# Performance work log

Hardware: AMD Instinct MI355X
Metric: run time of the kernel (lower is better)

Reference implementation:

```python
import jax, jax.numpy as jnp
import numpy as np

NUM_HEADS = 8
IN_CH = 512
SCALING = float(IN_CH // 8) ** (-0.5)  # 0.125, as in the torch module


def _conv1x1(x, w, b):
    # x: [B,C,H,W], w: [O,C], b: [O]  (1x1 conv == channel matmul)
    return jnp.einsum('bchw,oc->bohw', x, w) + b[None, :, None, None]


def setup_inputs() -> dict:
    key = jax.random.key(0)
    ks = jax.random.split(key, 9)
    B, C, H, W = 4, IN_CH, 96, 96
    q = jax.random.normal(ks[0], (B, C, H, W), jnp.float32)
    v = jax.random.normal(ks[1], (B, C, H, W), jnp.float32)
    # xavier_uniform for [C,C] 1x1 conv weights
    limit = float(np.sqrt(6.0 / (C + C)))
    Wq = jax.random.uniform(ks[2], (C, C), jnp.float32, -limit, limit)
    Wk = jax.random.uniform(ks[3], (C, C), jnp.float32, -limit, limit)
    Wv = jax.random.uniform(ks[4], (C, C), jnp.float32, -limit, limit)
    bq = jnp.zeros((C,), jnp.float32)
    bk = jnp.zeros((C,), jnp.float32)
    bv = jnp.zeros((C,), jnp.float32)
    # gamma is init to 0 in the module; use a nonzero value so the output is nontrivial
    gamma = jax.random.normal(ks[5], (1,), jnp.float32) * 0.1
    return {'q': q, 'v': v, 'Wq': Wq, 'bq': bq, 'Wk': Wk, 'bk': bk,
            'Wv': Wv, 'bv': bv, 'gamma': gamma}


def reference(q, v, Wq, bq, Wk, bk, Wv, bv, gamma):
    B, C, H, W = q.shape
    nh = NUM_HEADS
    hd = C // nh
    t = _conv1x1(q, Wq, bq) * SCALING           # proj_query
    f = _conv1x1(q, Wk, bk)                     # proj_key
    g = _conv1x1(v, Wv, bv)                     # proj_value
    t = t.reshape(B * nh, hd, H, W)
    f = f.reshape(B * nh, hd, H, W)
    g = g.reshape(B * nh, hd, H, W)
    # criss-cross affinity: row (same y, all x') and column (same x, all y'!=y)
    e_row = jnp.einsum('bdyx,bdyi->byxi', t, f)  # [Bh, H, W, W]
    e_col = jnp.einsum('bdyx,bdix->byxi', t, f)  # [Bh, H, W, H]
    # exclude the current position from the column branch (CUDA kernel skips i==y)
    diag = (jnp.arange(H)[:, None, None] == jnp.arange(H)[None, None, :])  # [H,1,H]
    e_col = jnp.where(diag, -jnp.inf, e_col)
    attn = jax.nn.softmax(jnp.concatenate([e_row, e_col], axis=-1), axis=-1)  # [Bh,H,W,W+H]
    a_row, a_col = attn[..., :W], attn[..., W:]
    out = (jnp.einsum('byxi,bdyi->bdyx', a_row, g)
           + jnp.einsum('byxi,bdix->bdyx', a_col, g))  # [Bh, hd, H, W]
    out = out.reshape(B, C, H, W)
    return gamma[0] * out + v
```

## Files before the change

kernel.cpp:

```cpp
#include <hip/hip_runtime.h>
#include <hip/hip_bf16.h>

typedef __bf16 bf16;
typedef __attribute__((ext_vector_type(8))) __bf16 bf16x8;
typedef __attribute__((ext_vector_type(4))) float floatx4;

#define B_  4
#define C_  512
#define H_  96
#define W_  96
#define HD_ 64
#define HW_ 9216
#define BH_ 32
#define SCALING_ 0.125f
#define BHS_ 589824

static constexpr size_t T_ELEMS = (size_t)BH_ * HD_ * HW_;
static constexpr size_t S_ELEMS = (size_t)BH_ * HW_;

__global__ __launch_bounds__(256) void cast_qv(
    const float* __restrict__ q, const float* __restrict__ v,
    const float* __restrict__ Wq, const float* __restrict__ Wk, const float* __restrict__ Wv,
    bf16* __restrict__ qbT, bf16* __restrict__ vbT, bf16* __restrict__ Wb)
{
    const int z = blockIdx.z;
    const int tid = threadIdx.x;

    if (z == 8) {
        const int bi = blockIdx.y * 144 + blockIdx.x;
        if (bi < 768) {
            const int i  = bi * 256 + tid;
            const int e0 = i * 4;
            const int arr = e0 >> 18;
            const int off = e0 & 262143;
            const float* W = (arr == 0) ? Wq : (arr == 1) ? Wk : Wv;
            const float4 val = *(const float4*)(W + off);
            bf16 tmp[4] __attribute__((aligned(8)));
            tmp[0] = (bf16)val.x; tmp[1] = (bf16)val.y;
            tmp[2] = (bf16)val.z; tmp[3] = (bf16)val.w;
            *(uint2*)(Wb + e0) = *(const uint2*)tmp;
        }
        return;
    }

    const int s = z >> 2, b = z & 3;
    const float* sb = (s ? v : q) + (size_t)b * C_ * HW_;
    bf16*       db = (s ? vbT : qbT) + (size_t)b * HW_ * C_;
    const int p0 = blockIdx.x * 64, c0 = blockIdx.y * 64;

    __shared__ float ts[64][65];

    for (int i = tid; i < 1024; i += 256) {
        const int row = i >> 4, seg = i & 15;
        const float4 val = *(const float4*)(sb + (size_t)(c0 + row) * HW_ + p0 + seg * 4);
        ts[row][seg * 4 + 0] = val.x; ts[row][seg * 4 + 1] = val.y;
        ts[row][seg * 4 + 2] = val.z; ts[row][seg * 4 + 3] = val.w;
    }
    __syncthreads();
    for (int i = tid; i < 512; i += 256) {
        const int prow = i >> 3, cseg = i & 7;
        bf16 tmp[8] __attribute__((aligned(16)));
        #pragma unroll
        for (int k = 0; k < 8; k++) tmp[k] = (bf16)ts[cseg * 8 + k][prow];
        *(uint4*)(db + (size_t)(p0 + prow) * C_ + c0 + cseg * 8) = *(const uint4*)tmp;
    }
}

__device__ __forceinline__ void stage_swz(
    const bf16* __restrict__ A, const bf16* __restrict__ Bsrc,
    int o0, int p0, int k0, int tid, bf16* As, bf16* Bs)
{
    #pragma unroll
    for (int c = tid; c < 512; c += 256) {
        const int sc = c ^ ((c >> 3) & 7);
        const int row = sc >> 2, seg = sc & 3;
        const bf16* gA = A    + (size_t)(o0 + row) * C_ + k0 + seg * 8;
        const bf16* gB = Bsrc + (size_t)(p0 + row) * C_ + k0 + seg * 8;
#if __has_builtin(__builtin_amdgcn_global_load_lds)
        char* lA = (char*)As + (size_t)(c & ~63) * 16;
        char* lB = (char*)Bs + (size_t)(c & ~63) * 16;
        __builtin_amdgcn_global_load_lds((const __attribute__((address_space(1))) void*)gA,
                                         (__attribute__((address_space(3))) void*)lA, 16, 0, 0);
        __builtin_amdgcn_global_load_lds((const __attribute__((address_space(1))) void*)gB,
                                         (__attribute__((address_space(3))) void*)lB, 16, 0, 0);
#else
        *(uint4*)((char*)As + (size_t)c * 16) = *(const uint4*)gA;
        *(uint4*)((char*)Bs + (size_t)c * 16) = *(const uint4*)gB;
#endif
    }
}

__device__ __forceinline__ int swz_chunk(int r, int quad)
{
    return (r * 4 + quad) ^ ((r >> 1) & 7);
}

__device__ __forceinline__ void compute_swz(
    const bf16* As, const bf16* Bs,
    int mrow, int ncol, int l16, int quad, floatx4 acc[4][4])
{
    bf16x8 af[4], bf_[4];
    #pragma unroll
    for (int i = 0; i < 4; i++)
        af[i] = *(const bf16x8*)&As[swz_chunk(mrow + i * 16 + l16, quad) * 8];
    #pragma unroll
    for (int j = 0; j < 4; j++)
        bf_[j] = *(const bf16x8*)&Bs[swz_chunk(ncol + j * 16 + l16, quad) * 8];
    #pragma unroll
    for (int i = 0; i < 4; i++)
        #pragma unroll
        for (int j = 0; j < 4; j++)
            acc[i][j] = __builtin_amdgcn_mfma_f32_16x16x32_bf16(af[i], bf_[j], acc[i][j], 0, 0, 0);
}

__global__ __launch_bounds__(256) void conv_mfma(
    const bf16* __restrict__ Wb,
    const float* __restrict__ bq, const float* __restrict__ bk, const float* __restrict__ bv,
    const bf16* __restrict__ qbT, const bf16* __restrict__ vbT,
    bf16* __restrict__ tR, bf16* __restrict__ fR, bf16* __restrict__ g)
{
    const int z = blockIdx.z, arr = z >> 2, b = z & 3;
    const bf16* A    = Wb + (size_t)arr * C_ * C_;
    const bf16* Bsrc = ((arr == 2) ? vbT : qbT) + (size_t)b * HW_ * C_;
    const float* bias = (arr == 0) ? bq : (arr == 1) ? bk : bv;
    const float scale = (arr == 0) ? SCALING_ : 1.0f;

    const int p0 = blockIdx.x * 128;
    const int o0 = blockIdx.y * 128;

    __shared__ __align__(16) bf16 smem[17408];
    bf16* const As0 = smem;
    bf16* const Bs0 = smem + 4096;
    bf16* const As1 = smem + 8192;
    bf16* const Bs1 = smem + 12288;

    const int tid = threadIdx.x, lane = tid & 63;
    const int wave = tid >> 6, l16 = lane & 15, quad = lane >> 4;
    const int mrow = (wave >> 1) * 64, ncol = (wave & 1) * 64;

    floatx4 acc[4][4] = {};

    stage_swz(A, Bsrc, o0, p0, 0, tid, As0, Bs0);
    __syncthreads();

    for (int k0 = 0; k0 < C_; k0 += 64) {
        if (k0 + 32 < C_) stage_swz(A, Bsrc, o0, p0, k0 + 32, tid, As1, Bs1);
        compute_swz(As0, Bs0, mrow, ncol, l16, quad, acc);
        __syncthreads();
        if (k0 + 64 < C_) stage_swz(A, Bsrc, o0, p0, k0 + 64, tid, As0, Bs0);
        compute_swz(As1, Bs1, mrow, ncol, l16, quad, acc);
        __syncthreads();
    }

    if (arr < 2) {
        #pragma unroll
        for (int i = 0; i < 4; i++)
            #pragma unroll
            for (int r = 0; r < 4; r++) {
                const int ol_ = mrow + i * 16 + quad * 4 + r;
                const float bi = bias[o0 + ol_];
                #pragma unroll
                for (int j = 0; j < 4; j++) {
                    const int pl = ncol + j * 16 + l16;
                    smem[pl * 128 + (ol_ ^ ((pl & 7) << 3))] = (bf16)((acc[i][j][r] + bi) * scale);
                }
            }
        __syncthreads();
        bf16* dst = (arr == 0) ? tR : fR;
        #pragma unroll
        for (int c = tid; c < 2048; c += 256) {
            const int pl = c >> 4, oo = c & 15;
            const int pg = p0 + pl;
            const int y = pg / 96, x = pg - y * 96;
            const int og = o0 + oo * 8;
            const int bh = b * 8 + (og >> 6), d = og & 63;
            const size_t di = (size_t)bh * BHS_ + (size_t)y * 6144 + x * 64 + d;
            *(uint4*)(dst + di) = *(const uint4*)&smem[pl * 128 + ((oo ^ (pl & 7)) * 8)];
        }
    } else {
        const int TS = 136;
        #pragma unroll
        for (int i = 0; i < 4; i++)
            #pragma unroll
            for (int r = 0; r < 4; r++) {
                const int ol_ = mrow + i * 16 + quad * 4 + r;
                const float bi = bias[o0 + ol_];
                #pragma unroll
                for (int j = 0; j < 4; j++) {
                    const int pl = ncol + j * 16 + l16;
                    smem[ol_ * TS + pl] = (bf16)(acc[i][j][r] + bi);
                }
            }
        __syncthreads();
        #pragma unroll
        for (int c = tid; c < 2048; c += 256) {
            const int ol_ = c >> 4, po = c & 15;
            const size_t di = (size_t)(b * 512 + o0 + ol_) * HW_ + p0 + po * 8;
            *(uint4*)(g + di) = *(const uint4*)&smem[ol_ * TS + po * 8];
        }
    }
}

__global__ __launch_bounds__(256) void transpose_g(const bf16* __restrict__ src, bf16* __restrict__ dst)
{
    const int plane = blockIdx.y;
    const int y0 = blockIdx.x * 32;
    const bf16* s = src + (size_t)plane * HW_;
    bf16*       d = dst + (size_t)plane * HW_;

    __shared__ bf16 ts[32][100];
    const int tid = threadIdx.x;

    #pragma unroll
    for (int i = tid; i < 768; i += 256) {
        const int row = i / 24, seg = i % 24;
        *(uint2*)&ts[row][seg * 4] = *(const uint2*)(s + (size_t)(y0 + row) * W_ + seg * 4);
    }
    __syncthreads();
    #pragma unroll
    for (int i = tid; i < 768; i += 256) {
        const int x = i >> 3, yseg = i & 7;
        bf16 tmp[4] __attribute__((aligned(8)));
        #pragma unroll
        for (int k = 0; k < 4; k++) tmp[k] = ts[yseg * 4 + k][x];
        *(uint2*)(d + (size_t)x * H_ + y0 + yseg * 4) = *(const uint2*)tmp;
    }
}

__global__ __launch_bounds__(512) void attn_col(
    const bf16* __restrict__ tR, const bf16* __restrict__ fR, const bf16* __restrict__ gT,
    bf16* __restrict__ outC, float* __restrict__ mc, float* __restrict__ lc)
{
    const int x = blockIdx.x;
    const int bh = blockIdx.y;

    __shared__ __align__(16) bf16 tl[96][72];
    __shared__ __align__(16) bf16 fl[96][72];
    __shared__ __align__(16) bf16 el[96][104];

    const int tid = threadIdx.x;
    const size_t sbase = (size_t)bh * BHS_;

    for (int i = tid; i < 768; i += 512) {
        const int y = i >> 3, oct = i & 7;
        const size_t gi = sbase + (size_t)y * 6144 + (size_t)x * 64 + oct * 8;
        *(uint4*)&tl[y][oct * 8] = *(const uint4*)(tR + gi);
        *(uint4*)&fl[y][oct * 8] = *(const uint4*)(fR + gi);
    }
    __syncthreads();

    const int lane = tid & 63, wave = tid >> 6;
    const int l16 = lane & 15, quad = lane >> 4;

    __builtin_amdgcn_s_setprio(1);
    #pragma unroll
    for (int it = 0; it < 5; it++) {
        const int idx = wave + it * 8;
        if (idx < 36) {
            const int mt = idx / 6, nt = idx % 6;
            floatx4 a = {};
            #pragma unroll
            for (int ks = 0; ks < 2; ks++) {
                bf16x8 af = *(const bf16x8*)&tl[mt * 16 + l16][ks * 32 + quad * 8];
                bf16x8 bf_ = *(const bf16x8*)&fl[nt * 16 + l16][ks * 32 + quad * 8];
                a = __builtin_amdgcn_mfma_f32_16x16x32_bf16(af, bf_, a, 0, 0, 0);
            }
            #pragma unroll
            for (int r = 0; r < 4; r++) {
                const int row = mt * 16 + quad * 4 + r, col = nt * 16 + l16;
                el[row][col] = (row == col) ? (bf16)(-1e30f) : (bf16)a[r];
            }
        }
    }
    __builtin_amdgcn_s_setprio(0);
    __syncthreads();

    bf16 (*gl)[104] = (bf16 (*)[104])fl;
    const size_t gbase = sbase + (size_t)x * 96;
    for (int i = tid; i < 768; i += 512) {
        const int d = i / 12, seg = i % 12;
        *(uint4*)&gl[d][seg * 8] = *(const uint4*)(gT + gbase + (size_t)d * HW_ + seg * 8);
    }

    if (tid < 384) {
        const int r = tid >> 2, qu = tid & 3;
        float vals[24];
        float m = -1e30f;
        #pragma unroll
        for (int k = 0; k < 3; k++) {
            bf16x8 v8 = *(const bf16x8*)&el[r][qu * 24 + k * 8];
            #pragma unroll
            for (int e = 0; e < 8; e++) { vals[k * 8 + e] = (float)v8[e]; m = fmaxf(m, vals[k * 8 + e]); }
        }
        m = fmaxf(m, __shfl_xor(m, 1));
        m = fmaxf(m, __shfl_xor(m, 2));
        float s = 0.f;
        #pragma unroll
        for (int k = 0; k < 3; k++) {
            bf16 tmp[8] __attribute__((aligned(16)));
            #pragma unroll
            for (int e = 0; e < 8; e++) {
                const float p = __expf(vals[k * 8 + e] - m);
                s += p; tmp[e] = (bf16)p;
            }
            *(uint4*)&el[r][qu * 24 + k * 8] = *(const uint4*)tmp;
        }
        s += __shfl_xor(s, 1);
        s += __shfl_xor(s, 2);
        if (qu == 0) {
            mc[(size_t)bh * HW_ + x * 96 + r] = m;
            lc[(size_t)bh * HW_ + x * 96 + r] = s;
        }
    }
    __syncthreads();

    bf16 (*ol)[72] = tl;
    __builtin_amdgcn_s_setprio(1);
    #pragma unroll
    for (int it = 0; it < 3; it++) {
        const int idx = wave + it * 8;
        const int mt = idx >> 2, nt = idx & 3;
        floatx4 a = {};
        #pragma unroll
        for (int ks = 0; ks < 3; ks++) {
            bf16x8 pf = *(const bf16x8*)&el[mt * 16 + l16][ks * 32 + quad * 8];
            bf16x8 gf = *(const bf16x8*)&gl[nt * 16 + l16][ks * 32 + quad * 8];
            a = __builtin_amdgcn_mfma_f32_16x16x32_bf16(pf, gf, a, 0, 0, 0);
        }
        #pragma unroll
        for (int r = 0; r < 4; r++)
            ol[mt * 16 + quad * 4 + r][nt * 16 + l16] = (bf16)a[r];
    }
    __builtin_amdgcn_s_setprio(0);
    __syncthreads();

    bf16* ob = outC + sbase + (size_t)x * 6144;
    for (int i = tid; i < 768; i += 512) {
        const int j = i >> 3, oct = i & 7;
        *(uint4*)(ob + (size_t)j * 64 + oct * 8) = *(const uint4*)&ol[j][oct * 8];
    }
}

__global__ __launch_bounds__(512) void attn_row_merge(
    const bf16* __restrict__ tR, const bf16* __restrict__ fR, const bf16* __restrict__ g,
    const bf16* __restrict__ outC, const float* __restrict__ mc, const float* __restrict__ lc,
    const float* __restrict__ v, const float* __restrict__ gamma, float* __restrict__ out)
{
    const int y = blockIdx.x;
    const int bh = blockIdx.y;

    __shared__ __align__(16) bf16 tl[96][72];
    __shared__ __align__(16) bf16 fl[96][72];
    __shared__ __align__(16) bf16 el[96][104];
    __shared__ float mll[96], lll[96], wrl[96], wcl[96];

    const int tid = threadIdx.x;
    const size_t sbase = (size_t)bh * BHS_;
    const size_t slice = sbase + (size_t)y * 6144;

    for (int i = tid; i < 768; i += 512) {
        const int j = i >> 3, oct = i & 7;
        *(uint4*)&tl[j][oct * 8] = *(const uint4*)(tR + slice + (size_t)j * 64 + oct * 8);
        *(uint4*)&fl[j][oct * 8] = *(const uint4*)(fR + slice + (size_t)j * 64 + oct * 8);
    }

    uint4 oc0, oc1 = {};
    {
        const int xx = tid >> 3, oct = tid & 7;
        oc0 = *(const uint4*)(outC + sbase + (size_t)xx * 6144 + (size_t)y * 64 + oct * 8);
    }
    if (tid < 256) {
        const int i1 = tid + 512, xx = i1 >> 3, oct = i1 & 7;
        oc1 = *(const uint4*)(outC + sbase + (size_t)xx * 6144 + (size_t)y * 64 + oct * 8);
    }
    float4 vpA, vpB = {}, vpC, vpD = {};
    {
        const int d = tid / 12, xf = tid - d * 12;
        const size_t ob = sbase + (size_t)d * HW_ + (size_t)y * 96 + xf * 4;
        vpA = *(const float4*)(v + ob);
        vpC = *(const float4*)(v + ob + 48);
    }
    if (tid < 256) {
        const int j = tid + 512;
        const int d = j / 12, xf = j - d * 12;
        const size_t ob = sbase + (size_t)d * HW_ + (size_t)y * 96 + xf * 4;
        vpB = *(const float4*)(v + ob);
        vpD = *(const float4*)(v + ob + 48);
    }
    float mcv = 0.f, lcv = 0.f;
    if (tid < 96) {
        mcv = mc[(size_t)bh * HW_ + tid * 96 + y];
        lcv = lc[(size_t)bh * HW_ + tid * 96 + y];
    }
    __syncthreads();

    const int lane = tid & 63, wave = tid >> 6;
    const int l16 = lane & 15, quad = lane >> 4;

    __builtin_amdgcn_s_setprio(1);
    #pragma unroll
    for (int it = 0; it < 5; it++) {
        const int idx = wave + it * 8;
        if (idx < 36) {
            const int mt = idx / 6, nt = idx % 6;
            floatx4 a = {};
            #pragma unroll
            for (int ks = 0; ks < 2; ks++) {
                bf16x8 af = *(const bf16x8*)&tl[mt * 16 + l16][ks * 32 + quad * 8];
                bf16x8 bf_ = *(const bf16x8*)&fl[nt * 16 + l16][ks * 32 + quad * 8];
                a = __builtin_amdgcn_mfma_f32_16x16x32_bf16(af, bf_, a, 0, 0, 0);
            }
            #pragma unroll
            for (int r = 0; r < 4; r++)
                el[mt * 16 + quad * 4 + r][nt * 16 + l16] = (bf16)a[r];
        }
    }
    __builtin_amdgcn_s_setprio(0);
    __syncthreads();

    bf16 (*gl)[104] = (bf16 (*)[104])tl;
    const size_t gbase = sbase + (size_t)y * 96;
    for (int i = tid; i < 768; i += 512) {
        const int d = i / 12, seg = i % 12;
        *(uint4*)&gl[d][seg * 8] = *(const uint4*)(g + gbase + (size_t)d * HW_ + seg * 8);
    }

    bf16 (*ocl)[72] = fl;
    {
        const int xx = tid >> 3, oct = tid & 7;
        *(uint4*)&ocl[xx][oct * 8] = oc0;
    }
    if (tid < 256) {
        const int i1 = tid + 512, xx = i1 >> 3, oct = i1 & 7;
        *(uint4*)&ocl[xx][oct * 8] = oc1;
    }

    if (tid < 384) {
        const int r = tid >> 2, qu = tid & 3;
        float vals[24];
        float m = -1e30f;
        #pragma unroll
        for (int k = 0; k < 3; k++) {
            bf16x8 v8 = *(const bf16x8*)&el[r][qu * 24 + k * 8];
            #pragma unroll
            for (int e = 0; e < 8; e++) { vals[k * 8 + e] = (float)v8[e]; m = fmaxf(m, vals[k * 8 + e]); }
        }
        m = fmaxf(m, __shfl_xor(m, 1));
        m = fmaxf(m, __shfl_xor(m, 2));
        float s = 0.f;
        #pragma unroll
        for (int k = 0; k < 3; k++) {
            bf16 tmp[8] __attribute__((aligned(16)));
            #pragma unroll
            for (int e = 0; e < 8; e++) {
                const float p = __expf(vals[k * 8 + e] - m);
                s += p; tmp[e] = (bf16)p;
            }
            *(uint4*)&el[r][qu * 24 + k * 8] = *(const uint4*)tmp;
        }
        s += __shfl_xor(s, 1);
        s += __shfl_xor(s, 2);
        if (qu == 0) { mll[r] = m; lll[r] = s; }
    }
    __syncthreads();

    if (tid < 96) {
        const float mrv = mll[tid], lrv = lll[tid];
        const float mm = fmaxf(mrv, mcv);
        const float wr = __expf(mrv - mm), wc = __expf(mcv - mm);
        const float dn = lrv * wr + lcv * wc;
        wrl[tid] = wr / dn;
        wcl[tid] = wc / dn;
    }
    floatx4 pa[3] = {};
    __builtin_amdgcn_s_setprio(1);
    #pragma unroll
    for (int it = 0; it < 3; it++) {
        const int idx = wave + it * 8;
        const int mt = idx >> 2, nt = idx & 3;
        #pragma unroll
        for (int ks = 0; ks < 3; ks++) {
            bf16x8 pf = *(const bf16x8*)&el[mt * 16 + l16][ks * 32 + quad * 8];
            bf16x8 gf = *(const bf16x8*)&gl[nt * 16 + l16][ks * 32 + quad * 8];
            pa[it] = __builtin_amdgcn_mfma_f32_16x16x32_bf16(pf, gf, pa[it], 0, 0, 0);
        }
    }
    __builtin_amdgcn_s_setprio(0);
    __syncthreads();

    #pragma unroll
    for (int it = 0; it < 3; it++) {
        const int idx = wave + it * 8;
        const int mt = idx >> 2, nt = idx & 3;
        #pragma unroll
        for (int r = 0; r < 4; r++)
            el[mt * 16 + quad * 4 + r][nt * 16 + l16] = (bf16)pa[it][r];
    }
    __syncthreads();

    const float gam = gamma[0];
    float* stage = (float*)&tl[0][0];

    #pragma unroll
    for (int h = 0; h < 2; h++) {
        const int xbase = h * 48;
        #pragma unroll
        for (int s = 0; s < 6; s++) {
            const int j = tid + s * 512;
            const int r = j >> 6, d = j & 63;
            const int xx = xbase + r;
            stage[r * 65 + d] = (float)el[xx][d] * wrl[xx] + (float)ocl[xx][d] * wcl[xx];
        }
        __syncthreads();
        {
            const int d = tid / 12, xf = tid - d * 12;
            float4 o4;
            o4.x = stage[(xf * 4 + 0) * 65 + d];
            o4.y = stage[(xf * 4 + 1) * 65 + d];
            o4.z = stage[(xf * 4 + 2) * 65 + d];
            o4.w = stage[(xf * 4 + 3) * 65 + d];
            const float4 vp = h ? vpC : vpA;
            float4 rr;
            rr.x = gam * o4.x + vp.x; rr.y = gam * o4.y + vp.y;
            rr.z = gam * o4.z + vp.z; rr.w = gam * o4.w + vp.w;
            const size_t ob = sbase + (size_t)d * HW_ + (size_t)y * 96 + xbase + xf * 4;
            *(float4*)(out + ob) = rr;
        }
        if (tid < 256) {
            const int j = tid + 512;
            const int d = j / 12, xf = j - d * 12;
            float4 o4;
            o4.x = stage[(xf * 4 + 0) * 65 + d];
            o4.y = stage[(xf * 4 + 1) * 65 + d];
            o4.z = stage[(xf * 4 + 2) * 65 + d];
            o4.w = stage[(xf * 4 + 3) * 65 + d];
            const float4 vp = h ? vpD : vpB;
            float4 rr;
            rr.x = gam * o4.x + vp.x; rr.y = gam * o4.y + vp.y;
            rr.z = gam * o4.z + vp.z; rr.w = gam * o4.w + vp.w;
            const size_t ob = sbase + (size_t)d * HW_ + (size_t)y * 96 + xbase + xf * 4;
            *(float4*)(out + ob) = rr;
        }
        __syncthreads();
    }
}

extern "C" void kernel_launch(void* const* d_in, const int* in_sizes, int n_in,
                              void* d_out, int out_size, void* d_ws, size_t ws_size,
                              hipStream_t stream)
{
    const float* q     = (const float*)d_in[0];
    const float* v     = (const float*)d_in[1];
    const float* Wq    = (const float*)d_in[2];
    const float* bq    = (const float*)d_in[3];
    const float* Wk    = (const float*)d_in[4];
    const float* bk    = (const float*)d_in[5];
    const float* Wv    = (const float*)d_in[6];
    const float* bv    = (const float*)d_in[7];
    const float* gamma = (const float*)d_in[8];
    float* out = (float*)d_out;

    char* w = (char*)d_ws;
    const size_t Tb = T_ELEMS * sizeof(bf16);
    bf16* qbT  = (bf16*)(w + 0 * Tb);
    bf16* vbT  = (bf16*)(w + 1 * Tb);
    bf16* tR   = (bf16*)(w + 2 * Tb);
    bf16* fR   = (bf16*)(w + 3 * Tb);
    bf16* g    = (bf16*)(w + 4 * Tb);
    bf16* gT   = (bf16*)(w + 1 * Tb);
    bf16* outC = (bf16*)(w + 0 * Tb);
    bf16* Wb   = (bf16*)(w + 6 * Tb);
    float* mc  = (float*)(w + 6 * Tb + 1572864);
    float* lc  = mc + S_ELEMS;

    cast_qv <<<dim3(144, 8, 9), 256, 0, stream>>>(q, v, Wq, Wk, Wv, qbT, vbT, Wb);
    conv_mfma<<<dim3(72, 4, 12), 256, 0, stream>>>(Wb, bq, bk, bv, qbT, vbT, tR, fR, g);
    transpose_g<<<dim3(3, 2048), 256, 0, stream>>>(g, gT);
    attn_col<<<dim3(96, BH_), 512, 0, stream>>>(tR, fR, gT, outC, mc, lc);
    attn_row_merge<<<dim3(96, BH_), 512, 0, stream>>>(tR, fR, g, outC, mc, lc, v, gamma, out);
}
```

Before: 379.9 us.

## Enlarge conv GEMM tiles to 256x256 with 8 waves and deeper async LDS pipeline

```diff
diff --git a/kernel.cpp b/kernel.cpp
--- a/kernel.cpp
+++ b/kernel.cpp
@@ -66,54 +66,27 @@
     }
 }
 
-__device__ __forceinline__ void stage_swz(
-    const bf16* __restrict__ A, const bf16* __restrict__ Bsrc,
-    int o0, int p0, int k0, int tid, bf16* As, bf16* Bs)
-{
-    #pragma unroll
-    for (int c = tid; c < 512; c += 256) {
+__device__ __forceinline__ int swz_chunk(int r, int quad)
+{
+    return (r * 4 + quad) ^ ((r >> 1) & 7);
+}
+
+__device__ __forceinline__ void stage_half(
+    const bf16* __restrict__ src, int row0, int k0, int tid, bf16* dst)
+{
+    #pragma unroll
+    for (int it = 0; it < 2; ++it) {
+        const int c  = tid + it * 512;
         const int sc = c ^ ((c >> 3) & 7);
         const int row = sc >> 2, seg = sc & 3;
-        const bf16* gA = A    + (size_t)(o0 + row) * C_ + k0 + seg * 8;
-        const bf16* gB = Bsrc + (size_t)(p0 + row) * C_ + k0 + seg * 8;
-#if __has_builtin(__builtin_amdgcn_global_load_lds)
-        char* lA = (char*)As + (size_t)(c & ~63) * 16;
-        char* lB = (char*)Bs + (size_t)(c & ~63) * 16;
-        __builtin_amdgcn_global_load_lds((const __attribute__((address_space(1))) void*)gA,
-                                         (__attribute__((address_space(3))) void*)lA, 16, 0, 0);
-        __builtin_amdgcn_global_load_lds((const __attribute__((address_space(1))) void*)gB,
-                                         (__attribute__((address_space(3))) void*)lB, 16, 0, 0);
-#else
-        *(uint4*)((char*)As + (size_t)c * 16) = *(const uint4*)gA;
-        *(uint4*)((char*)Bs + (size_t)c * 16) = *(const uint4*)gB;
-#endif
-    }
-}
-
-__device__ __forceinline__ int swz_chunk(int r, int quad)
-{
-    return (r * 4 + quad) ^ ((r >> 1) & 7);
-}
-
-__device__ __forceinline__ void compute_swz(
-    const bf16* As, const bf16* Bs,
-    int mrow, int ncol, int l16, int quad, floatx4 acc[4][4])
-{
-    bf16x8 af[4], bf_[4];
-    #pragma unroll
-    for (int i = 0; i < 4; i++)
-        af[i] = *(const bf16x8*)&As[swz_chunk(mrow + i * 16 + l16, quad) * 8];
-    #pragma unroll
-    for (int j = 0; j < 4; j++)
-        bf_[j] = *(const bf16x8*)&Bs[swz_chunk(ncol + j * 16 + l16, quad) * 8];
-    #pragma unroll
-    for (int i = 0; i < 4; i++)
-        #pragma unroll
-        for (int j = 0; j < 4; j++)
-            acc[i][j] = __builtin_amdgcn_mfma_f32_16x16x32_bf16(af[i], bf_[j], acc[i][j], 0, 0, 0);
-}
-
-__global__ __launch_bounds__(256) void conv_mfma(
+        const bf16* gp = src + (size_t)(row0 + row) * C_ + k0 + seg * 8;
+        char* lp = (char*)dst + (size_t)(c & ~63) * 16;
+        __builtin_amdgcn_global_load_lds((const __attribute__((address_space(1))) void*)gp,
+                                         (__attribute__((address_space(3))) void*)lp, 16, 0, 0);
+    }
+}
+
+__global__ __launch_bounds__(512, 2) void conv_mfma(
     const bf16* __restrict__ Wb,
     const float* __restrict__ bq, const float* __restrict__ bk, const float* __restrict__ bv,
     const bf16* __restrict__ qbT, const bf16* __restrict__ vbT,
@@ -125,78 +98,124 @@
     const float* bias = (arr == 0) ? bq : (arr == 1) ? bk : bv;
     const float scale = (arr == 0) ? SCALING_ : 1.0f;
 
-    const int p0 = blockIdx.x * 128;
-    const int o0 = blockIdx.y * 128;
-
-    __shared__ __align__(16) bf16 smem[17408];
-    bf16* const As0 = smem;
-    bf16* const Bs0 = smem + 4096;
-    bf16* const As1 = smem + 8192;
-    bf16* const Bs1 = smem + 12288;
+    const int p0 = blockIdx.x * 256;
+    const int o0 = blockIdx.y * 256;
+
+    __shared__ __align__(16) bf16 smem[65536];
 
     const int tid = threadIdx.x, lane = tid & 63;
     const int wave = tid >> 6, l16 = lane & 15, quad = lane >> 4;
-    const int mrow = (wave >> 1) * 64, ncol = (wave & 1) * 64;
-
-    floatx4 acc[4][4] = {};
-
-    stage_swz(A, Bsrc, o0, p0, 0, tid, As0, Bs0);
-    __syncthreads();
-
-    for (int k0 = 0; k0 < C_; k0 += 64) {
-        if (k0 + 32 < C_) stage_swz(A, Bsrc, o0, p0, k0 + 32, tid, As1, Bs1);
-        compute_swz(As0, Bs0, mrow, ncol, l16, quad, acc);
-        __syncthreads();
-        if (k0 + 64 < C_) stage_swz(A, Bsrc, o0, p0, k0 + 64, tid, As0, Bs0);
-        compute_swz(As1, Bs1, mrow, ncol, l16, quad, acc);
-        __syncthreads();
-    }
+    const int wr = wave >> 2, wc = wave & 3;
+
+    floatx4 acc[8][4] = {};
+
+    stage_half(A,    o0, 0,   tid, smem + 0);
+    stage_half(Bsrc, p0, 0,   tid, smem + 16384);
+    stage_half(A,    o0, 32,  tid, smem + 8192);
+    stage_half(Bsrc, p0, 32,  tid, smem + 24576);
+    stage_half(A,    o0, 64,  tid, smem + 32768);
+    stage_half(Bsrc, p0, 64,  tid, smem + 49152);
+
+    #pragma unroll
+    for (int t = 0; t < 8; t++) {
+        #pragma unroll
+        for (int qp = 0; qp < 4; qp++) {
+            if (qp == 0) {
+                if (t == 7) asm volatile("s_waitcnt vmcnt(0)" ::: "memory");
+                else        asm volatile("s_waitcnt vmcnt(4)" ::: "memory");
+                __builtin_amdgcn_sched_barrier(0);
+            }
+            __builtin_amdgcn_s_barrier();
+            __builtin_amdgcn_sched_barrier(0);
+
+            const int mg = qp & 1, ks = qp >> 1;
+            const bf16* Ak = smem + (size_t)(t & 1) * 32768 + (size_t)ks * 8192;
+            const bf16* Bk = Ak + 16384;
+
+            bf16x8 af[4], bf_[4];
+            #pragma unroll
+            for (int i = 0; i < 4; i++) {
+                const int r = wr * 128 + mg * 64 + i * 16 + l16;
+                af[i] = *(const bf16x8*)&Ak[swz_chunk(r, quad) * 8];
+            }
+            #pragma unroll
+            for (int j = 0; j < 4; j++) {
+                const int r = wc * 64 + j * 16 + l16;
+                bf_[j] = *(const bf16x8*)&Bk[swz_chunk(r, quad) * 8];
+            }
+
+            if (qp == 0 && t + 1 < 8)
+                stage_half(A,    o0, (t + 1) * 64 + 32, tid,
+                           smem + (size_t)((t + 1) & 1) * 32768 + 8192);
+            if (qp == 1 && t + 1 < 8)
+                stage_half(Bsrc, p0, (t + 1) * 64 + 32, tid,
+                           smem + (size_t)((t + 1) & 1) * 32768 + 24576);
+            if (qp == 2 && t + 2 < 8)
+                stage_half(A,    o0, (t + 2) * 64, tid,
+                           smem + (size_t)(t & 1) * 32768);
+            if (qp == 3 && t + 2 < 8)
+                stage_half(Bsrc, p0, (t + 2) * 64, tid,
+                           smem + (size_t)(t & 1) * 32768 + 16384);
+
+            asm volatile("s_waitcnt lgkmcnt(0)" ::: "memory");
+            __builtin_amdgcn_sched_barrier(0);
+
+            __builtin_amdgcn_s_setprio(1);
+            #pragma unroll
+            for (int i = 0; i < 4; i++)
+                #pragma unroll
+                for (int j = 0; j < 4; j++)
+                    acc[mg * 4 + i][j] =
+                        __builtin_amdgcn_mfma_f32_16x16x32_bf16(af[i], bf_[j], acc[mg * 4 + i][j], 0, 0, 0);
+            __builtin_amdgcn_s_setprio(0);
+        }
+    }
+    __syncthreads();
 
     if (arr < 2) {
         #pragma unroll
-        for (int i = 0; i < 4; i++)
-            #pragma unroll
-            for (int r = 0; r < 4; r++) {
-                const int ol_ = mrow + i * 16 + quad * 4 + r;
+        for (int mi = 0; mi < 8; mi++)
+            #pragma unroll
+            for (int rr = 0; rr < 4; rr++) {
+                const int ol_ = wr * 128 + mi * 16 + quad * 4 + rr;
                 const float bi = bias[o0 + ol_];
                 #pragma unroll
                 for (int j = 0; j < 4; j++) {
-                    const int pl = ncol + j * 16 + l16;
-                    smem[pl * 128 + (ol_ ^ ((pl & 7) << 3))] = (bf16)((acc[i][j][r] + bi) * scale);
+                    const int pl = wc * 64 + j * 16 + l16;
+                    smem[pl * 256 + (ol_ ^ ((pl & 7) << 3))] = (bf16)((acc[mi][j][rr] + bi) * scale);
                 }
             }
         __syncthreads();
         bf16* dst = (arr == 0) ? tR : fR;
         #pragma unroll
-        for (int c = tid; c < 2048; c += 256) {
-            const int pl = c >> 4, oo = c & 15;
+        for (int c = tid; c < 8192; c += 512) {
+            const int pl = c >> 5, oo = c & 31;
             const int pg = p0 + pl;
             const int y = pg / 96, x = pg - y * 96;
             const int og = o0 + oo * 8;
             const int bh = b * 8 + (og >> 6), d = og & 63;
             const size_t di = (size_t)bh * BHS_ + (size_t)y * 6144 + x * 64 + d;
-            *(uint4*)(dst + di) = *(const uint4*)&smem[pl * 128 + ((oo ^ (pl & 7)) * 8)];
+            *(uint4*)(dst + di) = *(const uint4*)&smem[pl * 256 + ((oo * 8) ^ ((pl & 7) << 3))];
         }
     } else {
-        const int TS = 136;
-        #pragma unroll
-        for (int i = 0; i < 4; i++)
-            #pragma unroll
-            for (int r = 0; r < 4; r++) {
-                const int ol_ = mrow + i * 16 + quad * 4 + r;
+        #pragma unroll
+        for (int mi = 0; mi < 8; mi++)
+            #pragma unroll
+            for (int rr = 0; rr < 4; rr++) {
+                const int ol_ = wr * 128 + mi * 16 + quad * 4 + rr;
                 const float bi = bias[o0 + ol_];
                 #pragma unroll
                 for (int j = 0; j < 4; j++) {
-                    const int pl = ncol + j * 16 + l16;
-                    smem[ol_ * TS + pl] = (bf16)(acc[i][j][r] + bi);
+                    const int pl = wc * 64 + j * 16 + l16;
+                    smem[ol_ * 256 + (pl ^ ((ol_ & 7) << 3))] = (bf16)(acc[mi][j][rr] + bi);
                 }
             }
         __syncthreads();
         #pragma unroll
-        for (int c = tid; c < 2048; c += 256) {
-            const int ol_ = c >> 4, po = c & 15;
+        for (int c = tid; c < 8192; c += 512) {
+            const int ol_ = c >> 5, po = c & 31;
             const size_t di = (size_t)(b * 512 + o0 + ol_) * HW_ + p0 + po * 8;
-            *(uint4*)(g + di) = *(const uint4*)&smem[ol_ * TS + po * 8];
+            *(uint4*)(g + di) = *(const uint4*)&smem[ol_ * 256 + ((po * 8) ^ ((ol_ & 7) << 3))];
         }
     }
 }
@@ -574,7 +593,7 @@
     float* lc  = mc + S_ELEMS;
 
     cast_qv <<<dim3(144, 8, 9), 256, 0, stream>>>(q, v, Wq, Wk, Wv, qbT, vbT, Wb);
-    conv_mfma<<<dim3(72, 4, 12), 256, 0, stream>>>(Wb, bq, bk, bv, qbT, vbT, tR, fR, g);
+    conv_mfma<<<dim3(36, 2, 12), 512, 0, stream>>>(Wb, bq, bk, bv, qbT, vbT, tR, fR, g);
     transpose_g<<<dim3(3, 2048), 256, 0, stream>>>(g, gT);
     attn_col<<<dim3(96, BH_), 512, 0, stream>>>(tR, fR, gT, outC, mc, lc);
     attn_row_merge<<<dim3(96, BH_), 512, 0, stream>>>(tR, fR, g, outC, mc, lc, v, gamma, out);
```

Result: slower. 393.1 us (+3.5%).
